# Performance work log

Hardware: AMD Instinct MI355X
Metric: run time of the kernel (lower is better)

Reference implementation:

```python
import jax, jax.numpy as jnp
import numpy as np
from math import floor, ceil

B, CIN, COUT, H, W, K = 1, 8, 8, 1024, 1024, 31


def setup_inputs() -> dict:
    key = jax.random.key(0)
    k1, k2, k3 = jax.random.split(key, 3)
    signal = jax.random.normal(k1, (B, CIN, H, W), dtype=jnp.float32)
    weight = jax.random.normal(k2, (COUT, CIN, K, K), dtype=jnp.float32)
    bias = jax.random.normal(k3, (COUT,), dtype=jnp.float32)
    return {"signal": signal, "weight": weight, "bias": bias}


def reference(signal, weight, bias):
    # FFT-based cross-correlation with padding='same', stride=1, dilation=1, groups=1
    kh, kw = weight.shape[2], weight.shape[3]
    ph, pw = (kh - 1) / 2, (kw - 1) / 2
    # 'same' padding: floor/ceil split per side (torch f.pad order: last dim first)
    s = jnp.pad(signal, ((0, 0), (0, 0), (floor(ph), ceil(ph)), (floor(pw), ceil(pw))))
    Hs, Ws = s.shape[2], s.shape[3]  # padded signal size used for the output crop
    # torch pads last dim to even length for rfft efficiency
    if s.shape[3] % 2 != 0:
        s = jnp.pad(s, ((0, 0), (0, 0), (0, 0), (0, 1)))
    # zero-pad kernel up to the (even-padded) signal size
    kpad = jnpp = jnp.pad(weight, ((0, 0), (0, 0), (0, s.shape[2] - kh), (0, s.shape[3] - kw)))
    sig_fr = jnp.fft.rfftn(s, axes=(2, 3))            # [B, Cin, Hs, Wf]
    ker_fr = jnp.conj(jnp.fft.rfftn(kpad, axes=(2, 3)))  # conj -> cross-correlation
    out_fr = sig_fr * ker_fr                           # broadcast: [Cout, Cin, Hs, Wf] (B==1)
    out = jnp.fft.irfftn(out_fr, axes=(2, 3))          # [Cout, Cin, Hs, Ws_even]
    out = out[:, :, : Hs - kh + 1, : Ws - kw + 1]      # valid crop (stride 1)
    # bias.view(1, -1, 1, 1): broadcasts over dim1 (== Cin == Cout here)
    return out + bias.reshape(1, -1, 1, 1)
```

## Files before the change

### kernel.cpp

```cpp
#include <hip/hip_runtime.h>


typedef _Float16 f16x8 __attribute__((ext_vector_type(8)));
typedef float    f32x4 __attribute__((ext_vector_type(4)));

#define TY   16
#define TXB  64
#define SR   46
#define SDW  48
#define SROW 52

__device__ unsigned int g_wA[8 * 31 * 256];

__global__ void wpack(const float* __restrict__ wgt) {
  int t = blockIdx.x * 256 + threadIdx.x;
  if (t >= 8 * 31 * 256) return;
  const int d  = t & 3;
  const int m  = (t >> 2) & 15;
  const int kg = (t >> 6) & 3;
  const int r  = t >> 8;
  const int i  = r % 31;
  const int c  = r / 31;
  const int o  = m & 7;
  const int s  = m >> 3;
  const int k0 = kg * 8 + 2 * d;
  const int j0 = k0 - s, j1 = k0 + 1 - s;
  const float* wsrc = wgt + ((o * 8 + c) * 31 + i) * 31;
  const float w0 = ((unsigned)j0 < 31u) ? wsrc[j0] : 0.f;
  const float w1 = ((unsigned)j1 < 31u) ? wsrc[j1] : 0.f;
  union { _Float16 h[2]; unsigned int u; } p;
  p.h[0] = (_Float16)w0; p.h[1] = (_Float16)w1;
  g_wA[t] = p.u;
}

__global__ __launch_bounds__(256, 4)
void conv_mfma2(const float* __restrict__ sig,
                const float* __restrict__ bias,
                float* __restrict__ out) {
  __shared__ __align__(16) unsigned int ldss[SR * SROW];

  const int tid = threadIdx.x;
  const int c  = blockIdx.z;
  const int x0 = blockIdx.x * TXB;
  const int y0 = blockIdx.y * TY;

  const float* sc = sig + c * (1024 * 1024);
  for (int f = tid; f < SR * SDW; f += 256) {
    const int r = f / SDW;
    const int d = f - r * SDW;
    const int gy = y0 + r - 15;
    const int gx = x0 + 2 * d - 15;
    float s0 = 0.f, s1 = 0.f;
    if ((unsigned)gy < 1024u) {
      const float* srcr = sc + gy * 1024;
      if ((unsigned)gx < 1024u)       s0 = srcr[gx];
      if ((unsigned)(gx + 1) < 1024u) s1 = srcr[gx + 1];
    }
    union { _Float16 h[2]; unsigned int u; } p;
    p.h[0] = (_Float16)s0; p.h[1] = (_Float16)s1;
    ldss[r * SROW + d] = p.u;
  }
  __syncthreads();

  const int lane = tid & 63;
  const int wv   = tid >> 6;
  const int n    = lane & 15;
  const int kg   = lane >> 4;
  const int xw   = wv * 16;

  f32x4 acc[8];
  #pragma unroll
  for (int xg = 0; xg < 8; ++xg) acc[xg] = (f32x4){0.f, 0.f, 0.f, 0.f};

  const uint4* wq = (const uint4*)g_wA + c * (31 * 64) + lane;
  uint4 wnext = wq[0];

  for (int i = 0; i < 31; ++i) {
    union { uint4 v; f16x8 h; } au;
    au.v = wnext;
    if (i < 30) wnext = wq[(i + 1) * 64];

    const unsigned int* rowp = &ldss[(n + i) * SROW + 8 * wv + 4 * kg];
    const uint4 R0 = *(const uint4*)(rowp);
    const uint4 R1 = *(const uint4*)(rowp + 4);
    const uint4 R2 = *(const uint4*)(rowp + 8);
    const unsigned int W[12] = {R0.x, R0.y, R0.z, R0.w,
                                R1.x, R1.y, R1.z, R1.w,
                                R2.x, R2.y, R2.z, R2.w};
    #pragma unroll
    for (int xg = 0; xg < 8; ++xg) {
      union { unsigned int u[4]; f16x8 h; } b;
      b.u[0] = W[xg]; b.u[1] = W[xg + 1]; b.u[2] = W[xg + 2]; b.u[3] = W[xg + 3];
      acc[xg] = __builtin_amdgcn_mfma_f32_16x16x32_f16(au.h, b.h, acc[xg], 0, 0, 0);
    }
  }

  const float bv  = bias[c];
  const int  h    = kg >> 1;
  const int  olo  = (kg & 1) * 4;
  const int  y    = y0 + n;
  const bool low  = (kg < 2);

  #pragma unroll
  for (int r = 0; r < 4; ++r) {
    float av[8], pv[8];
    #pragma unroll
    for (int xg = 0; xg < 8; ++xg) {
      av[xg] = acc[xg][r] + bv;
      pv[xg] = __shfl_xor(av[xg], 32);
    }
    const int o = olo + r;
    float* op = out + (((size_t)(o * 8 + c) * 1024 + y) * 1024 + x0 + xw + 8 * h);
    float4 v0, v1;
    if (h == 0) {
      v0.x = low ? av[0] : pv[0]; v0.y = low ? pv[0] : av[0];
      v0.z = low ? av[1] : pv[1]; v0.w = low ? pv[1] : av[1];
      v1.x = low ? av[2] : pv[2]; v1.y = low ? pv[2] : av[2];
      v1.z = low ? av[3] : pv[3]; v1.w = low ? pv[3] : av[3];
    } else {
      v0.x = low ? av[4] : pv[4]; v0.y = low ? pv[4] : av[4];
      v0.z = low ? av[5] : pv[5]; v0.w = low ? pv[5] : av[5];
      v1.x = low ? av[6] : pv[6]; v1.y = low ? pv[6] : av[6];
      v1.z = low ? av[7] : pv[7]; v1.w = low ? pv[7] : av[7];
    }
    *(float4*)(op)     = v0;
    *(float4*)(op + 4) = v1;
  }
}

extern "C" void kernel_launch(void* const* d_in, const int* in_sizes, int n_in,
                              void* d_out, int out_size, void* d_ws, size_t ws_size,
                              hipStream_t stream) {
  const float* sig  = (const float*)d_in[0];
  const float* wgt  = (const float*)d_in[1];
  const float* bias = (const float*)d_in[2];
  float* out = (float*)d_out;

  wpack<<<(8 * 31 * 256 + 255) / 256, 256, 0, stream>>>(wgt);
  dim3 grid(1024 / TXB, 1024 / TY, 8);
  conv_mfma2<<<grid, 256, 0, stream>>>(sig, bias, out);
}
```

Baseline: 410.0 us.

## Remap MFMA tile to rows and hold a rolling register window of LDS rows

Re-maps the MFMA so the N dimension indexes output columns and the M dimension indexes output-channel/row-shift pairs. The kernel now keeps a 16-row register window of packed signal columns, reused across eight row-pair accumulators, and refills one row per tap row. LDS stores a second shifted copy of the f16 pairs so odd column offsets read directly, which doubles LDS footprint and uses an odd row stride to avoid bank conflicts. This is meant to cut per-MFMA LDS reads. The cost is much higher register pressure and scalar uncoalesced-ish output stores instead of float4 stores.

```diff
diff --git a/kernel.cpp b/kernel.cpp
--- a/kernel.cpp
+++ b/kernel.cpp
@@ -6,38 +6,41 @@
 
 #define TY   16
 #define TXB  64
-#define SR   46
+#define SR   48
 #define SDW  48
-#define SROW 52
+#define SROW 97
 
-__device__ unsigned int g_wA[8 * 31 * 256];
+__device__ unsigned int g_wA[8 * 32 * 64 * 4];
 
 __global__ void wpack(const float* __restrict__ wgt) {
   int t = blockIdx.x * 256 + threadIdx.x;
-  if (t >= 8 * 31 * 256) return;
-  const int d  = t & 3;
-  const int m  = (t >> 2) & 15;
-  const int kg = (t >> 6) & 3;
-  const int r  = t >> 8;
-  const int i  = r % 31;
-  const int c  = r / 31;
+  if (t >= 8 * 32 * 64 * 4) return;
+  const int d    = t & 3;
+  const int lane = (t >> 2) & 63;
+  const int i    = (t >> 8) & 31;
+  const int c    = t >> 13;
+  const int m  = lane & 15;
+  const int kg = lane >> 4;
   const int o  = m & 7;
   const int s  = m >> 3;
+  const int ip = i - s;
   const int k0 = kg * 8 + 2 * d;
-  const int j0 = k0 - s, j1 = k0 + 1 - s;
-  const float* wsrc = wgt + ((o * 8 + c) * 31 + i) * 31;
-  const float w0 = ((unsigned)j0 < 31u) ? wsrc[j0] : 0.f;
-  const float w1 = ((unsigned)j1 < 31u) ? wsrc[j1] : 0.f;
+  float w0 = 0.f, w1 = 0.f;
+  if ((unsigned)ip < 31u) {
+    const float* wsrc = wgt + ((o * 8 + c) * 31 + ip) * 31;
+    if (k0 < 31)     w0 = wsrc[k0];
+    if (k0 + 1 < 31) w1 = wsrc[k0 + 1];
+  }
   union { _Float16 h[2]; unsigned int u; } p;
   p.h[0] = (_Float16)w0; p.h[1] = (_Float16)w1;
   g_wA[t] = p.u;
 }
 
 __global__ __launch_bounds__(256, 4)
-void conv_mfma2(const float* __restrict__ sig,
+void conv_mfma3(const float* __restrict__ sig,
                 const float* __restrict__ bias,
                 float* __restrict__ out) {
-  __shared__ __align__(16) unsigned int ldss[SR * SROW];
+  __shared__ unsigned int ldss[SR * SROW];
 
   const int tid = threadIdx.x;
   const int c  = blockIdx.z;
@@ -45,20 +48,23 @@
   const int y0 = blockIdx.y * TY;
 
   const float* sc = sig + c * (1024 * 1024);
-  for (int f = tid; f < SR * SDW; f += 256) {
+  for (int f = tid; f < 46 * SDW; f += 256) {
     const int r = f / SDW;
     const int d = f - r * SDW;
     const int gy = y0 + r - 15;
     const int gx = x0 + 2 * d - 15;
-    float s0 = 0.f, s1 = 0.f;
+    float s0 = 0.f, s1 = 0.f, s2 = 0.f;
     if ((unsigned)gy < 1024u) {
       const float* srcr = sc + gy * 1024;
       if ((unsigned)gx < 1024u)       s0 = srcr[gx];
       if ((unsigned)(gx + 1) < 1024u) s1 = srcr[gx + 1];
+      if ((unsigned)(gx + 2) < 1024u) s2 = srcr[gx + 2];
     }
-    union { _Float16 h[2]; unsigned int u; } p;
-    p.h[0] = (_Float16)s0; p.h[1] = (_Float16)s1;
-    ldss[r * SROW + d] = p.u;
+    union { _Float16 h[2]; unsigned int u; } p0, p1;
+    p0.h[0] = (_Float16)s0; p0.h[1] = (_Float16)s1;
+    p1.h[0] = (_Float16)s1; p1.h[1] = (_Float16)s2;
+    ldss[r * SROW + d]       = p0.u;
+    ldss[r * SROW + SDW + d] = p1.u;
   }
   __syncthreads();
 
@@ -68,63 +74,62 @@
   const int kg   = lane >> 4;
   const int xw   = wv * 16;
 
+  const int E = xw + n + 8 * kg;
+  const unsigned int* lbase = ldss + (E & 1) * SDW + (E >> 1);
+
   f32x4 acc[8];
   #pragma unroll
-  for (int xg = 0; xg < 8; ++xg) acc[xg] = (f32x4){0.f, 0.f, 0.f, 0.f};
+  for (int p = 0; p < 8; ++p) acc[p] = (f32x4){0.f, 0.f, 0.f, 0.f};
 
-  const uint4* wq = (const uint4*)g_wA + c * (31 * 64) + lane;
-  uint4 wnext = wq[0];
+  unsigned int Bc[16][4];
+  #pragma unroll
+  for (int r = 0; r < 16; ++r) {
+    const unsigned int* q = lbase + r * SROW;
+    Bc[r][0] = q[0]; Bc[r][1] = q[1]; Bc[r][2] = q[2]; Bc[r][3] = q[3];
+  }
 
-  for (int i = 0; i < 31; ++i) {
-    union { uint4 v; f16x8 h; } au;
-    au.v = wnext;
-    if (i < 30) wnext = wq[(i + 1) * 64];
+  const uint4* wq = (const uint4*)g_wA + (size_t)c * (32 * 64) + lane;
+  uint4 aq = wq[0];
 
-    const unsigned int* rowp = &ldss[(n + i) * SROW + 8 * wv + 4 * kg];
-    const uint4 R0 = *(const uint4*)(rowp);
-    const uint4 R1 = *(const uint4*)(rowp + 4);
-    const uint4 R2 = *(const uint4*)(rowp + 8);
-    const unsigned int W[12] = {R0.x, R0.y, R0.z, R0.w,
-                                R1.x, R1.y, R1.z, R1.w,
-                                R2.x, R2.y, R2.z, R2.w};
+  for (int ib = 0; ib < 2; ++ib) {
     #pragma unroll
-    for (int xg = 0; xg < 8; ++xg) {
-      union { unsigned int u[4]; f16x8 h; } b;
-      b.u[0] = W[xg]; b.u[1] = W[xg + 1]; b.u[2] = W[xg + 2]; b.u[3] = W[xg + 3];
-      acc[xg] = __builtin_amdgcn_mfma_f32_16x16x32_f16(au.h, b.h, acc[xg], 0, 0, 0);
+    for (int u = 0; u < 16; ++u) {
+      const int i = ib * 16 + u;
+      union { uint4 v; f16x8 h; } au;
+      au.v = aq;
+      if (i < 31) aq = wq[(i + 1) * 64];
+
+      {
+        union { unsigned int uu[4]; f16x8 h; } b;
+        b.uu[0] = Bc[u][0]; b.uu[1] = Bc[u][1]; b.uu[2] = Bc[u][2]; b.uu[3] = Bc[u][3];
+        acc[0] = __builtin_amdgcn_mfma_f32_16x16x32_f16(au.h, b.h, acc[0], 0, 0, 0);
+      }
+      {
+        const unsigned int* q = lbase + (i + 16) * SROW;
+        Bc[u][0] = q[0]; Bc[u][1] = q[1]; Bc[u][2] = q[2]; Bc[u][3] = q[3];
+      }
+      #pragma unroll
+      for (int p = 1; p < 8; ++p) {
+        const int sl = (u + 2 * p) & 15;
+        union { unsigned int uu[4]; f16x8 h; } b;
+        b.uu[0] = Bc[sl][0]; b.uu[1] = Bc[sl][1]; b.uu[2] = Bc[sl][2]; b.uu[3] = Bc[sl][3];
+        acc[p] = __builtin_amdgcn_mfma_f32_16x16x32_f16(au.h, b.h, acc[p], 0, 0, 0);
+      }
     }
   }
 
-  const float bv  = bias[c];
-  const int  h    = kg >> 1;
-  const int  olo  = (kg & 1) * 4;
-  const int  y    = y0 + n;
-  const bool low  = (kg < 2);
-
+  const float bv = bias[c];
+  const int s   = kg >> 1;
+  const int ob  = (kg & 1) * 4;
+  const int xs  = x0 + xw + n;
   #pragma unroll
-  for (int r = 0; r < 4; ++r) {
-    float av[8], pv[8];
+  for (int p = 0; p < 8; ++p) {
+    const int y = y0 + 2 * p + s;
     #pragma unroll
-    for (int xg = 0; xg < 8; ++xg) {
-      av[xg] = acc[xg][r] + bv;
-      pv[xg] = __shfl_xor(av[xg], 32);
+    for (int r = 0; r < 4; ++r) {
+      const int o = ob + r;
+      out[(((size_t)(o * 8 + c) * 1024 + y) * 1024) + xs] = acc[p][r] + bv;
     }
-    const int o = olo + r;
-    float* op = out + (((size_t)(o * 8 + c) * 1024 + y) * 1024 + x0 + xw + 8 * h);
-    float4 v0, v1;
-    if (h == 0) {
-      v0.x = low ? av[0] : pv[0]; v0.y = low ? pv[0] : av[0];
-      v0.z = low ? av[1] : pv[1]; v0.w = low ? pv[1] : av[1];
-      v1.x = low ? av[2] : pv[2]; v1.y = low ? pv[2] : av[2];
-      v1.z = low ? av[3] : pv[3]; v1.w = low ? pv[3] : av[3];
-    } else {
-      v0.x = low ? av[4] : pv[4]; v0.y = low ? pv[4] : av[4];
-      v0.z = low ? av[5] : pv[5]; v0.w = low ? pv[5] : av[5];
-      v1.x = low ? av[6] : pv[6]; v1.y = low ? pv[6] : av[6];
-      v1.z = low ? av[7] : pv[7]; v1.w = low ? pv[7] : av[7];
-    }
-    *(float4*)(op)     = v0;
-    *(float4*)(op + 4) = v1;
   }
 }
 
@@ -136,7 +141,7 @@
   const float* bias = (const float*)d_in[2];
   float* out = (float*)d_out;
 
-  wpack<<<(8 * 31 * 256 + 255) / 256, 256, 0, stream>>>(wgt);
+  wpack<<<(8 * 32 * 64 * 4 + 255) / 256, 256, 0, stream>>>(wgt);
   dim3 grid(1024 / TXB, 1024 / TY, 8);
-  conv_mfma2<<<grid, 256, 0, stream>>>(sig, bias, out);
+  conv_mfma3<<<grid, 256, 0, stream>>>(sig, bias, out);
 }
```

After: 397.9 us. -3.0%, faster.
